# Performance work log

Measured on AMD Instinct MI355X. Metric: run time of the kernel, lower is better.

Reference implementation:

```python
import jax, jax.numpy as jnp
import numpy as np
from jax import lax


def setup_inputs() -> dict:
    key = jax.random.key(0)
    ks = jax.random.split(key, 16)
    B, T, F = 32, 32, 64
    H, N, A, C = 256, 1024, 64, 192
    M = A + C  # overall_memory_size
    s = 0.05  # weight scale (xavier-like magnitude)
    inp = {
        "batch": jax.random.normal(ks[0], (B, T, F), jnp.float32),
        "Wi": jax.random.normal(ks[1], (3, H, F), jnp.float32) * s,
        "bi": jax.random.normal(ks[2], (3, H, 1), jnp.float32) * s,
        "Wh": jax.random.normal(ks[3], (3, H, H), jnp.float32) * s,
        "bh": jax.random.normal(ks[4], (3, H, 1), jnp.float32) * s,
        "Wm": jax.random.normal(ks[5], (3, H, M), jnp.float32) * s,
        "bm": jax.random.normal(ks[6], (3, H, 1), jnp.float32) * s,
        "W_output": jax.random.normal(ks[7], (10, H), jnp.float32) * s,
        "b_output": jnp.full((10, 1), 0.1, jnp.float32),
        "memory_addresses": jax.random.normal(ks[8], (N, A), jnp.float32) * s,
        "W_query": jax.random.normal(ks[9], (M, H), jnp.float32) * s,
        "b_query": jax.random.normal(ks[10], (M, 1), jnp.float32) * s,
        "u_sharpen": jax.random.normal(ks[11], (1, H), jnp.float32) * s,
        "W_content_hidden": jax.random.normal(ks[12], (C, H), jnp.float32) * s,
        "W_content_input": jax.random.normal(ks[13], (C, F), jnp.float32) * s,
    }
    return inp


def reference(batch, Wi, bi, Wh, bh, Wm, bm, W_output, b_output,
              memory_addresses, W_query, b_query, u_sharpen,
              W_content_hidden, W_content_input):
    B, T, F = batch.shape
    H = Wh.shape[1]
    N, A = memory_addresses.shape
    C = W_content_hidden.shape[0]

    # faithful to torch: batch[:, t, :].reshape(F, B) per step (raw reshape, not transpose)
    xs = jnp.transpose(batch, (1, 0, 2)).reshape(T, F, B)  # [T, F, B]

    h0 = jnp.zeros((H, B), batch.dtype)
    content0 = jnp.zeros((B, N, C), batch.dtype)
    addr = jnp.broadcast_to(memory_addresses, (B, N, A))

    def step(carry, x):
        h, content = carry  # h: [H,B], content: [B,N,C]
        full = jnp.concatenate([addr, content], axis=-1)  # [B,N,M]
        # content-based addressing with sharpening
        q = W_query @ h + b_query                          # [M,B]
        sim = jnp.einsum('bnm,mb->nb', full, q)            # [N,B]
        beta = jax.nn.softplus(u_sharpen @ h) + 1.0        # [1,B]
        w = jax.nn.softmax(beta * sim, axis=0)             # [N,B]
        # read (before update, as in step_on_batch_element)
        reading = jnp.einsum('bnm,nb->mb', full, w)        # [M,B]
        # write: additive ReLU candidate
        cand = jax.nn.relu(W_content_hidden @ h + W_content_input @ x)  # [C,B]
        content = content + jnp.einsum('nb,cb->bnc', w, cand)
        # CustomGRU: gate order [r, z, n]
        gi = jnp.einsum('ghf,fb->ghb', Wi, x) + bi
        gh = jnp.einsum('ghk,kb->ghb', Wh, h) + bh
        gm = jnp.einsum('ghm,mb->ghb', Wm, reading) + bm
        r = jax.nn.sigmoid(gi[0] + gh[0] + gm[0])
        z = jax.nn.sigmoid(gi[1] + gh[1] + gm[1])
        n = jnp.tanh(gi[2] + gm[2] + r * gh[2])
        h_new = (1.0 - z) * n + z * h
        out = jax.nn.log_softmax(W_output @ h_new + b_output, axis=0)  # [10,B]
        return (h_new, content), (h_new, out)

    _, (hs, outs) = lax.scan(step, (h0, content0), xs)
    return hs, outs  # [T,H,B], [T,10,B]
```

## Files before the change

kernel.cpp:

```cpp
#include <hip/hip_runtime.h>

typedef unsigned int u32;
typedef unsigned short u16;
typedef _Float16 f16x2 __attribute__((ext_vector_type(2)));


#define WP_A0    0
#define WP_A1    40960
#define WP_A2H   81920
#define WP_A2I   114688
#define WP_AQ    122880
#define WP_AC    155648
#define WP_AM    186368
#define WP_AT2   284672
#define WP_M4    317440
#define WP_WO4   350208

#define SH_HX   0
#define SH_H2   256
#define SH_Q    416
#define SH_Q2   672
#define SH_GA0  704
#define SH_GA1  960
#define SH_GH2  1216
#define SH_GI2  1472
#define SH_GM   1728
#define SH_SIMA 2496
#define SH_R2   3520
#define SH_D    3648
#define SH_G    3680
#define SH_RED  3712
#define SH_RED2 3728
#define SH_MISC 3744
#define SH_B10  3752
#define SH_RA   3768
#define SH_CAND 4280
#define SH_W    7352
#define SMEM_FLOATS 23736
#define SMEM_BYTES (SMEM_FLOATS*4)

#define WRED(v) { v += __shfl_xor(v,32); v += __shfl_xor(v,16); v += __shfl_xor(v,8); \
                  v += __shfl_xor(v,4);  v += __shfl_xor(v,2);  v += __shfl_xor(v,1); }

__device__ __forceinline__ f16x2 bch2(u32 u) { return __builtin_bit_cast(f16x2, u); }

#if __has_builtin(__builtin_amdgcn_fdot2)
__device__ __forceinline__ float FDOT2(u32 a, u32 b, float c) {
  return __builtin_amdgcn_fdot2(bch2(a), bch2(b), c, false);
}
#else
__device__ __forceinline__ float FDOT2(u32 a, u32 b, float c) {
  f16x2 x = bch2(a), y = bch2(b);
  return c + (float)x[0]*(float)y[0] + (float)x[1]*(float)y[1];
}
#endif

__device__ __forceinline__ u16 f2h(float x) {
  _Float16 h = (_Float16)x; return __builtin_bit_cast(u16, h);
}
__device__ __forceinline__ float h2f(u16 u) {
  return (float)__builtin_bit_cast(_Float16, u);
}
__device__ __forceinline__ u32 packh2(float lo, float hi) {
  return (u32)f2h(lo) | ((u32)f2h(hi) << 16);
}

template<int NK4>
__device__ __forceinline__ float mv_os4(const u32* __restrict__ Wb,
                                        const u32* __restrict__ c2, const int ln)
{
  const uint4* wp = (const uint4*)Wb + ln;
  const uint4* c4 = (const uint4*)c2;
  uint4 w0 = wp[0], w1 = wp[64];
  uint4 c0 = c4[0], c1 = c4[1];
  wp += 128;
  float a0 = 0.f, a1 = 0.f, a2 = 0.f, a3 = 0.f;
  #pragma unroll 1
  for (int it = 0; it < NK4/2 - 1; ++it) {
    const uint4 nw0 = wp[0], nw1 = wp[64];
    const uint4 nc0 = c4[2*it + 2], nc1 = c4[2*it + 3];
    wp += 128;
    a0 = FDOT2(w0.x, c0.x, a0);
    a1 = FDOT2(w0.y, c0.y, a1);
    a2 = FDOT2(w0.z, c0.z, a2);
    a3 = FDOT2(w0.w, c0.w, a3);
    a0 = FDOT2(w1.x, c1.x, a0);
    a1 = FDOT2(w1.y, c1.y, a1);
    a2 = FDOT2(w1.z, c1.z, a2);
    a3 = FDOT2(w1.w, c1.w, a3);
    w0 = nw0; w1 = nw1; c0 = nc0; c1 = nc1;
  }
  a0 = FDOT2(w0.x, c0.x, a0);
  a1 = FDOT2(w0.y, c0.y, a1);
  a2 = FDOT2(w0.z, c0.z, a2);
  a3 = FDOT2(w0.w, c0.w, a3);
  a0 = FDOT2(w1.x, c1.x, a0);
  a1 = FDOT2(w1.y, c1.y, a1);
  a2 = FDOT2(w1.z, c1.z, a2);
  a3 = FDOT2(w1.w, c1.w, a3);
  return (a0 + a1) + (a2 + a3);
}

__device__ __forceinline__ void out_lse(const float* __restrict__ b10,
    float* __restrict__ out, const int t_out, const int bb, const int ln)
{
  float v = (ln < 10) ? b10[ln] : -1e30f;
  float m = v;
  m = fmaxf(m, __shfl_xor(m, 8, 16));
  m = fmaxf(m, __shfl_xor(m, 4, 16));
  m = fmaxf(m, __shfl_xor(m, 2, 16));
  m = fmaxf(m, __shfl_xor(m, 1, 16));
  float e = (ln < 10) ? __expf(v - m) : 0.f;
  float s = e;
  s += __shfl_xor(s, 8, 16);
  s += __shfl_xor(s, 4, 16);
  s += __shfl_xor(s, 2, 16);
  s += __shfl_xor(s, 1, 16);
  if (ln < 10) out[262144 + t_out * 320 + ln * 32 + bb] = v - m - logf(s);
}

__device__ __forceinline__ void pack_panel(const float* __restrict__ srcA, int KA, int np4A,
                                           const float* __restrict__ srcB, int KB,
                                           int np4tot, int o0, u32* __restrict__ dstu, int tid)
{
  uint4* d4 = (uint4*)dstu;
  for (int idx = tid; idx < np4tot * 64; idx += 256) {
    const int k4 = idx >> 6, o = idx & 63;
    const float* s = (k4 < np4A) ? (srcA + (size_t)(o0 + o) * KA + k4 * 8)
                                 : (srcB + (size_t)(o0 + o) * KB + (k4 - np4A) * 8);
    uint4 v;
    v.x = packh2(s[0], s[1]); v.y = packh2(s[2], s[3]);
    v.z = packh2(s[4], s[5]); v.w = packh2(s[6], s[7]);
    d4[idx] = v;
  }
}

__global__ void pack_weights(const float* __restrict__ Wi, const float* __restrict__ Wh,
                             const float* __restrict__ Wm, const float* __restrict__ Wq,
                             const float* __restrict__ Wch, const float* __restrict__ Wci,
                             const float* __restrict__ maddr, const float* __restrict__ Wo,
                             u32* __restrict__ wsu)
{
  const int b = blockIdx.x, tid = threadIdx.x;
  if (b < 4)        pack_panel(Wh,          256, 32, Wi,        64, 40, b*64,      wsu + WP_A0  + b*10240, tid);
  else if (b < 8)   pack_panel(Wh + 65536,  256, 32, Wi + 16384,64, 40, (b-4)*64,  wsu + WP_A1  + (b-4)*10240, tid);
  else if (b < 12)  pack_panel(Wh + 131072, 256, 32, Wh,       256, 32, (b-8)*64,  wsu + WP_A2H + (b-8)*8192, tid);
  else if (b < 16)  pack_panel(Wi + 32768,   64,  8, Wi,        64,  8, (b-12)*64, wsu + WP_A2I + (b-12)*2048, tid);
  else if (b < 20)  pack_panel(Wq,          256, 32, Wq,       256, 32, (b-16)*64, wsu + WP_AQ  + (b-16)*8192, tid);
  else if (b < 23)  pack_panel(Wch,         256, 32, Wci,       64, 40, (b-20)*64, wsu + WP_AC  + (b-20)*10240, tid);
  else if (b < 35) { int x = b-23; int g = x>>2;
                    pack_panel(Wm + g*65536, 256, 32, Wm,      256, 32, (x&3)*64,  wsu + WP_AM  + x*8192, tid); }
  else if (b < 51)  pack_panel(maddr,        64,  8, maddr,     64,  8, (b-35)*64, wsu + WP_AT2 + (b-35)*2048, tid);
  else if (b < 55) {
    const int kb = b - 51;
    uint4* d4 = (uint4*)(wsu + WP_M4);
    for (int idx = tid; idx < 2048; idx += 256) {
      const int k4 = kb*32 + (idx >> 6), a = idx & 63;
      const float* s = maddr + (size_t)(8*k4)*64 + a;
      uint4 v;
      v.x = packh2(s[0],   s[64]);  v.y = packh2(s[128], s[192]);
      v.z = packh2(s[256], s[320]); v.w = packh2(s[384], s[448]);
      d4[k4*64 + a] = v;
    }
  } else {
    uint4* d4 = (uint4*)(wsu + WP_WO4);
    for (int idx = tid; idx < 320; idx += 256) {
      const int j = idx >> 5, l = idx & 31;
      const float* s = Wo + j*256 + l*8;
      uint4 v;
      v.x = packh2(s[0], s[1]); v.y = packh2(s[2], s[3]);
      v.z = packh2(s[4], s[5]); v.w = packh2(s[6], s[7]);
      d4[idx] = v;
    }
  }
}

__global__ __launch_bounds__(1024) void dntm_step(
    const float* __restrict__ batch, const float* __restrict__ bi,
    const float* __restrict__ bh, const float* __restrict__ bm,
    const float* __restrict__ bo, const float* __restrict__ bq,
    const float* __restrict__ usharp, const u32* __restrict__ wsu,
    float* __restrict__ out)
{
  extern __shared__ float sm[];
  u32* h2u   = (u32*)(sm + SH_H2);
  u32* Q2u   = (u32*)(sm + SH_Q2);
  u32* R2u   = (u32*)(sm + SH_R2);
  u16* candh = (u16*)(sm + SH_CAND);
  u16* SW16  = (u16*)(sm + SH_W);
  u32* SW32  = (u32*)(sm + SH_W);
  const int tid = threadIdx.x, ln = tid & 63, wv = tid >> 6;
  const int bb = blockIdx.x;

  if (tid < 256) sm[SH_HX + tid] = 0.f;
  if (tid < 128) h2u[tid] = 0u;
  if (tid >= 128 && tid < 160) {
    const int j = tid - 128;
    const int i0 = (2*j)*32 + bb, i1 = i0 + 32;
    const float x0 = batch[(i0 >> 6)*2048 + (i0 & 63)];
    const float x1 = batch[(i1 >> 6)*2048 + (i1 & 63)];
    h2u[128 + j] = packh2(x0, x1);
  }
  __syncthreads();

  for (int t = 0; t < 32; ++t) {
    if (wv < 4) {
      sm[SH_GA0 + wv*64 + ln] = mv_os4<40>(wsu + WP_A0 + wv*10240, h2u, ln);
    } else if (wv < 8) {
      const int p = wv - 4;
      sm[SH_GA1 + p*64 + ln] = mv_os4<40>(wsu + WP_A1 + p*10240, h2u, ln);
    } else if (wv < 12) {
      const int p = wv - 8;
      sm[SH_GH2 + p*64 + ln] = mv_os4<32>(wsu + WP_A2H + p*8192, h2u, ln);
      sm[SH_GI2 + p*64 + ln] = mv_os4<8> (wsu + WP_A2I + p*2048, h2u + 128, ln);
    } else if (wv == 12) {
      const float qa = mv_os4<32>(wsu + WP_AQ,        h2u, ln) + bq[ln];
      const float qb = mv_os4<32>(wsu + WP_AQ + 8192, h2u, ln) + bq[64 + ln];
      sm[SH_Q + ln] = qa; sm[SH_Q + 64 + ln] = qb;
      const float rh = __shfl_down(qa, 1);
      if (!(ln & 1)) Q2u[ln >> 1] = packh2(qa, rh);
    } else if (wv == 13) {
      sm[SH_Q + 128 + ln] = mv_os4<32>(wsu + WP_AQ + 16384, h2u, ln) + bq[128 + ln];
      sm[SH_Q + 192 + ln] = mv_os4<32>(wsu + WP_AQ + 24576, h2u, ln) + bq[192 + ln];
    } else if (wv == 14) {
      candh[t*192 +      ln] = f2h(fmaxf(mv_os4<40>(wsu + WP_AC,         h2u, ln), 0.f));
      candh[t*192 + 64 + ln] = f2h(fmaxf(mv_os4<40>(wsu + WP_AC + 10240, h2u, ln), 0.f));
    } else {
      candh[t*192 + 128 + ln] = f2h(fmaxf(mv_os4<40>(wsu + WP_AC + 20480, h2u, ln), 0.f));
      {
        const float4 h4 = *(const float4*)(sm + SH_HX + ln*4);
        const float4 u4 = *(const float4*)(usharp + ln*4);
        float v = h4.x*u4.x + h4.y*u4.y + h4.z*u4.z + h4.w*u4.w;
        WRED(v);
        if (!ln) sm[SH_MISC] = fmaxf(v, 0.f) + log1pf(expf(-fabsf(v))) + 1.f;
      }
      if (t > 0) {
        const uint4 ch = ((const uint4*)h2u)[ln & 31];
        const uint4* wo4 = (const uint4*)(wsu + WP_WO4);
        for (int j = 0; j < 10; ++j) {
          float lv = 0.f;
          if (ln < 32) {
            const uint4 w4 = wo4[j*32 + ln];
            lv = FDOT2(w4.x, ch.x, lv); lv = FDOT2(w4.y, ch.y, lv);
            lv = FDOT2(w4.z, ch.z, lv); lv = FDOT2(w4.w, ch.w, lv);
          }
          WRED(lv);
          if (!ln) sm[SH_B10 + j] = lv + bo[j];
        }
      }
    }
    __syncthreads();

    if (wv < 8) {
      sm[SH_SIMA + wv*128 + ln]      = mv_os4<8>(wsu + WP_AT2 + (2*wv)*2048,   Q2u, ln);
      sm[SH_SIMA + wv*128 + 64 + ln] = mv_os4<8>(wsu + WP_AT2 + (2*wv+1)*2048, Q2u, ln);
    } else if (wv < 15) {
      const float q0 = sm[SH_Q + 64 + ln], q1 = sm[SH_Q + 128 + ln], q2 = sm[SH_Q + 192 + ln];
      for (int s = wv - 8; s < t; s += 7) {
        float a2 = h2f(candh[s*192 + ln]) * q0
                 + h2f(candh[s*192 + 64 + ln]) * q1
                 + h2f(candh[s*192 + 128 + ln]) * q2;
        WRED(a2);
        if (!ln) sm[SH_D + s] = a2;
      }
    } else {
      if (t > 0) out_lse(sm + SH_B10, out, t - 1, bb, ln);
    }
    __syncthreads();

    const int n3 = wv * 64 + ln;
    float v = sm[SH_SIMA + n3];
    #pragma unroll 4
    for (int s = 0; s < t; ++s) v = fmaf(sm[SH_D + s], h2f(SW16[s*1024 + n3]), v);
    v *= sm[SH_MISC];
    {
      float mx = v;
      mx = fmaxf(mx, __shfl_xor(mx, 32)); mx = fmaxf(mx, __shfl_xor(mx, 16));
      mx = fmaxf(mx, __shfl_xor(mx, 8));  mx = fmaxf(mx, __shfl_xor(mx, 4));
      mx = fmaxf(mx, __shfl_xor(mx, 2));  mx = fmaxf(mx, __shfl_xor(mx, 1));
      if (!ln) sm[SH_RED + wv] = mx;
    }
    __syncthreads();

    {
      float gmx = sm[SH_RED];
      #pragma unroll
      for (int i = 1; i < 16; ++i) gmx = fmaxf(gmx, sm[SH_RED + i]);
      const float e = __expf(v - gmx);
      SW16[t*1024 + n3] = f2h(e);
      float s2 = e; WRED(s2);
      if (!ln) sm[SH_RED2 + wv] = s2;
    }
    __syncthreads();

    {
      float tot = 0.f;
      #pragma unroll
      for (int i = 0; i < 16; ++i) tot += sm[SH_RED2 + i];
      const float inv = 1.0f / tot;
      if (wv < 8) {
        const float acc = mv_os4<16>(wsu + WP_M4 + wv*16*256,
                                     SW32 + t*512 + wv*64, ln);
        sm[SH_RA + wv*64 + ln] = acc * inv;
      } else {
        const uint4 ea = ((const uint4*)(SW32 + t*512))[ln*2];
        const uint4 eb = ((const uint4*)(SW32 + t*512))[ln*2 + 1];
        for (int s = wv - 8; s < t; s += 8) {
          const uint4 wa = ((const uint4*)(SW32 + s*512))[ln*2];
          const uint4 wb = ((const uint4*)(SW32 + s*512))[ln*2 + 1];
          float a2 = 0.f;
          a2 = FDOT2(ea.x, wa.x, a2); a2 = FDOT2(ea.y, wa.y, a2);
          a2 = FDOT2(ea.z, wa.z, a2); a2 = FDOT2(ea.w, wa.w, a2);
          a2 = FDOT2(eb.x, wb.x, a2); a2 = FDOT2(eb.y, wb.y, a2);
          a2 = FDOT2(eb.z, wb.z, a2); a2 = FDOT2(eb.w, wb.w, a2);
          WRED(a2);
          if (!ln) sm[SH_G + s] = a2 * inv;
        }
      }
    }
    __syncthreads();

    if (wv == 0) {
      float r = 0.f;
      #pragma unroll
      for (int j = 0; j < 8; ++j) r += sm[SH_RA + j*64 + ln];
      const float rh = __shfl_down(r, 1);
      if (!(ln & 1)) R2u[ln >> 1] = packh2(r, rh);
    } else if (wv < 4) {
      const int c = (wv - 1)*64 + ln;
      float r = 0.f;
      for (int s = 0; s < t; ++s) r = fmaf(h2f(candh[s*192 + c]), sm[SH_G + s], r);
      const float rh = __shfl_down(r, 1);
      if (!(ln & 1)) R2u[wv*32 + (ln >> 1)] = packh2(r, rh);
    }
    __syncthreads();

    if (wv < 12) {
      const int g = wv >> 2, p = wv & 3;
      sm[SH_GM + g*256 + p*64 + ln] = mv_os4<32>(wsu + WP_AM + wv*8192, R2u, ln);
    } else if (wv < 14) {
      float tot = 0.f;
      #pragma unroll
      for (int i = 0; i < 16; ++i) tot += sm[SH_RED2 + i];
      const float inv = 1.0f / tot;
      u32* p = SW32 + t*512 + (wv - 12)*256 + ln*4;
      uint4 v4 = *(const uint4*)p;
      v4.x = packh2(h2f(v4.x & 0xffff)*inv, h2f(v4.x >> 16)*inv);
      v4.y = packh2(h2f(v4.y & 0xffff)*inv, h2f(v4.y >> 16)*inv);
      v4.z = packh2(h2f(v4.z & 0xffff)*inv, h2f(v4.z >> 16)*inv);
      v4.w = packh2(h2f(v4.w & 0xffff)*inv, h2f(v4.w >> 16)*inv);
      *(uint4*)p = v4;
    } else if (wv == 14) {
      if (t < 31 && ln < 32) {
        const int i0 = (2*ln)*32 + bb, i1 = i0 + 32;
        const float x0 = batch[(i0 >> 6)*2048 + (t+1)*64 + (i0 & 63)];
        const float x1 = batch[(i1 >> 6)*2048 + (t+1)*64 + (i1 & 63)];
        h2u[128 + ln] = packh2(x0, x1);
      }
    }
    __syncthreads();

    if (tid < 256) {
      const int h = tid;
      const float g0  = sm[SH_GA0 + h] + bi[h]       + bh[h]       + sm[SH_GM + h]       + bm[h];
      const float g1  = sm[SH_GA1 + h] + bi[256 + h] + bh[256 + h] + sm[SH_GM + 256 + h] + bm[256 + h];
      const float gh2v = sm[SH_GH2 + h] + bh[512 + h];
      const float gi2v = sm[SH_GI2 + h] + bi[512 + h];
      const float gm2  = sm[SH_GM + 512 + h] + bm[512 + h];
      const float r = 1.f / (1.f + __expf(-g0));
      const float z = 1.f / (1.f + __expf(-g1));
      const float nn = tanhf(gi2v + gm2 + r * gh2v);
      const float hn = (1.f - z) * nn + z * sm[SH_HX + h];
      sm[SH_HX + h] = hn;
      out[t*8192 + h*32 + bb] = hn;
      const float hn1 = __shfl_down(hn, 1);
      if (!(tid & 1)) h2u[tid >> 1] = packh2(hn, hn1);
    }
    __syncthreads();
  }

  if (wv == 0) {
    const uint4 ch = ((const uint4*)h2u)[ln & 31];
    const uint4* wo4 = (const uint4*)(wsu + WP_WO4);
    for (int j = 0; j < 10; ++j) {
      float lv = 0.f;
      if (ln < 32) {
        const uint4 w4 = wo4[j*32 + ln];
        lv = FDOT2(w4.x, ch.x, lv); lv = FDOT2(w4.y, ch.y, lv);
        lv = FDOT2(w4.z, ch.z, lv); lv = FDOT2(w4.w, ch.w, lv);
      }
      WRED(lv);
      if (!ln) sm[SH_B10 + j] = lv + bo[j];
    }
    out_lse(sm + SH_B10, out, 31, bb, ln);
  }
}

extern "C" void kernel_launch(void* const* d_in, const int* in_sizes, int n_in,
                              void* d_out, int out_size, void* d_ws, size_t ws_size,
                              hipStream_t stream) {
  (void)in_sizes; (void)n_in; (void)out_size; (void)ws_size;
  const float* batch = (const float*)d_in[0];
  const float* Wi    = (const float*)d_in[1];
  const float* bi    = (const float*)d_in[2];
  const float* Wh    = (const float*)d_in[3];
  const float* bh    = (const float*)d_in[4];
  const float* Wm    = (const float*)d_in[5];
  const float* bm    = (const float*)d_in[6];
  const float* Wo    = (const float*)d_in[7];
  const float* bo    = (const float*)d_in[8];
  const float* maddr = (const float*)d_in[9];
  const float* Wq    = (const float*)d_in[10];
  const float* bq    = (const float*)d_in[11];
  const float* us    = (const float*)d_in[12];
  const float* Wch   = (const float*)d_in[13];
  const float* Wci   = (const float*)d_in[14];
  u32* wsu  = (u32*)d_ws;
  float* out = (float*)d_out;

  hipFuncSetAttribute((const void*)dntm_step,
                      hipFuncAttributeMaxDynamicSharedMemorySize, 163840);

  pack_weights<<<56, 256, 0, stream>>>(Wi, Wh, Wm, Wq, Wch, Wci, maddr, Wo, wsu);
  dntm_step<<<32, 1024, SMEM_BYTES, stream>>>(batch, bi, bh, bm, bo, bq, us, wsu, out);
}
```

Before: 585.1 us.

## Rebalance per-wave matvec work and deepen load pipelining in fp16 dot helpers

Reassigns the first-phase matvecs across the 16 waves. The Wh n-gate product is split in two K-halves, spread over waves 0-7 and summed in the GRU stage. The candidate, query, input-gate and output-logit work is regrouped so no wave carries two full 40-group matvecs. The mv_os4 helper is fully unrolled with double-buffered groups of four uint4 loads, and a paired helper does two 8-group matvecs with interleaved loads. The goal is a shorter critical path per timestep, at the cost of more registers and an extra shared-memory partial buffer, with a launch-bounds hint added.

```diff
diff --git a/kernel.cpp b/kernel.cpp
--- a/kernel.cpp
+++ b/kernel.cpp
@@ -16,27 +16,28 @@
 #define WP_M4    317440
 #define WP_WO4   350208
 
-#define SH_HX   0
-#define SH_H2   256
-#define SH_Q    416
-#define SH_Q2   672
-#define SH_GA0  704
-#define SH_GA1  960
-#define SH_GH2  1216
-#define SH_GI2  1472
-#define SH_GM   1728
-#define SH_SIMA 2496
-#define SH_R2   3520
-#define SH_D    3648
-#define SH_G    3680
-#define SH_RED  3712
-#define SH_RED2 3728
-#define SH_MISC 3744
-#define SH_B10  3752
-#define SH_RA   3768
-#define SH_CAND 4280
-#define SH_W    7352
-#define SMEM_FLOATS 23736
+#define SH_HX    0
+#define SH_H2    256
+#define SH_Q     416
+#define SH_Q2    672
+#define SH_GA0   704
+#define SH_GA1   960
+#define SH_GH2A  1216
+#define SH_GH2B  1472
+#define SH_GI2   1728
+#define SH_GM    1984
+#define SH_SIMA  2752
+#define SH_R2    3776
+#define SH_D     3904
+#define SH_G     3936
+#define SH_RED   3968
+#define SH_RED2  3984
+#define SH_MISC  4000
+#define SH_B10   4008
+#define SH_RA    4024
+#define SH_CAND  4536
+#define SH_W     7608
+#define SMEM_FLOATS 23992
 #define SMEM_BYTES (SMEM_FLOATS*4)
 
 #define WRED(v) { v += __shfl_xor(v,32); v += __shfl_xor(v,16); v += __shfl_xor(v,8); \
@@ -69,36 +70,75 @@
 __device__ __forceinline__ float mv_os4(const u32* __restrict__ Wb,
                                         const u32* __restrict__ c2, const int ln)
 {
-  const uint4* wp = (const uint4*)Wb + ln;
-  const uint4* c4 = (const uint4*)c2;
-  uint4 w0 = wp[0], w1 = wp[64];
-  uint4 c0 = c4[0], c1 = c4[1];
-  wp += 128;
+  static_assert(NK4 % 4 == 0, "NK4 must be multiple of 4");
+  constexpr int NG = NK4 / 4;
+  const uint4* __restrict__ wp = (const uint4*)Wb + ln;
+  const uint4* __restrict__ c4 = (const uint4*)c2;
   float a0 = 0.f, a1 = 0.f, a2 = 0.f, a3 = 0.f;
-  #pragma unroll 1
-  for (int it = 0; it < NK4/2 - 1; ++it) {
-    const uint4 nw0 = wp[0], nw1 = wp[64];
-    const uint4 nc0 = c4[2*it + 2], nc1 = c4[2*it + 3];
-    wp += 128;
-    a0 = FDOT2(w0.x, c0.x, a0);
-    a1 = FDOT2(w0.y, c0.y, a1);
-    a2 = FDOT2(w0.z, c0.z, a2);
-    a3 = FDOT2(w0.w, c0.w, a3);
-    a0 = FDOT2(w1.x, c1.x, a0);
-    a1 = FDOT2(w1.y, c1.y, a1);
-    a2 = FDOT2(w1.z, c1.z, a2);
-    a3 = FDOT2(w1.w, c1.w, a3);
-    w0 = nw0; w1 = nw1; c0 = nc0; c1 = nc1;
-  }
-  a0 = FDOT2(w0.x, c0.x, a0);
-  a1 = FDOT2(w0.y, c0.y, a1);
-  a2 = FDOT2(w0.z, c0.z, a2);
-  a3 = FDOT2(w0.w, c0.w, a3);
-  a0 = FDOT2(w1.x, c1.x, a0);
-  a1 = FDOT2(w1.y, c1.y, a1);
-  a2 = FDOT2(w1.z, c1.z, a2);
-  a3 = FDOT2(w1.w, c1.w, a3);
+  uint4 wa0, wa1, wa2, wa3, ca0, ca1, ca2, ca3;
+  uint4 wb0, wb1, wb2, wb3, cb0, cb1, cb2, cb3;
+#define LWA_(g) { wa0 = wp[(g)*256]; wa1 = wp[(g)*256+64]; wa2 = wp[(g)*256+128]; wa3 = wp[(g)*256+192]; \
+                  ca0 = c4[(g)*4];   ca1 = c4[(g)*4+1];    ca2 = c4[(g)*4+2];     ca3 = c4[(g)*4+3]; }
+#define LWB_(g) { wb0 = wp[(g)*256]; wb1 = wp[(g)*256+64]; wb2 = wp[(g)*256+128]; wb3 = wp[(g)*256+192]; \
+                  cb0 = c4[(g)*4];   cb1 = c4[(g)*4+1];    cb2 = c4[(g)*4+2];     cb3 = c4[(g)*4+3]; }
+#define CMPA_ { a0=FDOT2(wa0.x,ca0.x,a0); a1=FDOT2(wa0.y,ca0.y,a1); a2=FDOT2(wa0.z,ca0.z,a2); a3=FDOT2(wa0.w,ca0.w,a3); \
+                a0=FDOT2(wa1.x,ca1.x,a0); a1=FDOT2(wa1.y,ca1.y,a1); a2=FDOT2(wa1.z,ca1.z,a2); a3=FDOT2(wa1.w,ca1.w,a3); \
+                a0=FDOT2(wa2.x,ca2.x,a0); a1=FDOT2(wa2.y,ca2.y,a1); a2=FDOT2(wa2.z,ca2.z,a2); a3=FDOT2(wa2.w,ca2.w,a3); \
+                a0=FDOT2(wa3.x,ca3.x,a0); a1=FDOT2(wa3.y,ca3.y,a1); a2=FDOT2(wa3.z,ca3.z,a2); a3=FDOT2(wa3.w,ca3.w,a3); }
+#define CMPB_ { a0=FDOT2(wb0.x,cb0.x,a0); a1=FDOT2(wb0.y,cb0.y,a1); a2=FDOT2(wb0.z,cb0.z,a2); a3=FDOT2(wb0.w,cb0.w,a3); \
+                a0=FDOT2(wb1.x,cb1.x,a0); a1=FDOT2(wb1.y,cb1.y,a1); a2=FDOT2(wb1.z,cb1.z,a2); a3=FDOT2(wb1.w,cb1.w,a3); \
+                a0=FDOT2(wb2.x,cb2.x,a0); a1=FDOT2(wb2.y,cb2.y,a1); a2=FDOT2(wb2.z,cb2.z,a2); a3=FDOT2(wb2.w,cb2.w,a3); \
+                a0=FDOT2(wb3.x,cb3.x,a0); a1=FDOT2(wb3.y,cb3.y,a1); a2=FDOT2(wb3.z,cb3.z,a2); a3=FDOT2(wb3.w,cb3.w,a3); }
+  LWA_(0);
+  if constexpr (NG == 1) {
+    CMPA_;
+  } else {
+    LWB_(1);
+    #pragma unroll
+    for (int g = 0; g + 2 < NG; ++g) {
+      if ((g & 1) == 0) { CMPA_; LWA_(g + 2); }
+      else              { CMPB_; LWB_(g + 2); }
+    }
+    if constexpr (((NG - 2) & 1) == 0) { CMPA_; CMPB_; }
+    else                               { CMPB_; CMPA_; }
+  }
+#undef LWA_
+#undef LWB_
+#undef CMPA_
+#undef CMPB_
   return (a0 + a1) + (a2 + a3);
+}
+
+__device__ __forceinline__ float2 mv2_os4_8(const u32* __restrict__ W0,
+    const u32* __restrict__ W1, const u32* __restrict__ c2, const int ln)
+{
+  const uint4* __restrict__ w0p = (const uint4*)W0 + ln;
+  const uint4* __restrict__ w1p = (const uint4*)W1 + ln;
+  const uint4* __restrict__ c4 = (const uint4*)c2;
+  float a0=0.f,a1=0.f,a2=0.f,a3=0.f, b0=0.f,b1=0.f,b2=0.f,b3=0.f;
+  uint4 wa0=w0p[0],   wa1=w0p[64],  wa2=w0p[128], wa3=w0p[192];
+  uint4 ca0=c4[0],    ca1=c4[1],    ca2=c4[2],    ca3=c4[3];
+  uint4 wb0=w0p[256], wb1=w0p[320], wb2=w0p[384], wb3=w0p[448];
+  uint4 cb0=c4[4],    cb1=c4[5],    cb2=c4[6],    cb3=c4[7];
+  a0=FDOT2(wa0.x,ca0.x,a0); a1=FDOT2(wa0.y,ca0.y,a1); a2=FDOT2(wa0.z,ca0.z,a2); a3=FDOT2(wa0.w,ca0.w,a3);
+  a0=FDOT2(wa1.x,ca1.x,a0); a1=FDOT2(wa1.y,ca1.y,a1); a2=FDOT2(wa1.z,ca1.z,a2); a3=FDOT2(wa1.w,ca1.w,a3);
+  a0=FDOT2(wa2.x,ca2.x,a0); a1=FDOT2(wa2.y,ca2.y,a1); a2=FDOT2(wa2.z,ca2.z,a2); a3=FDOT2(wa2.w,ca2.w,a3);
+  a0=FDOT2(wa3.x,ca3.x,a0); a1=FDOT2(wa3.y,ca3.y,a1); a2=FDOT2(wa3.z,ca3.z,a2); a3=FDOT2(wa3.w,ca3.w,a3);
+  wa0=w1p[0]; wa1=w1p[64]; wa2=w1p[128]; wa3=w1p[192];
+  a0=FDOT2(wb0.x,cb0.x,a0); a1=FDOT2(wb0.y,cb0.y,a1); a2=FDOT2(wb0.z,cb0.z,a2); a3=FDOT2(wb0.w,cb0.w,a3);
+  a0=FDOT2(wb1.x,cb1.x,a0); a1=FDOT2(wb1.y,cb1.y,a1); a2=FDOT2(wb1.z,cb1.z,a2); a3=FDOT2(wb1.w,cb1.w,a3);
+  a0=FDOT2(wb2.x,cb2.x,a0); a1=FDOT2(wb2.y,cb2.y,a1); a2=FDOT2(wb2.z,cb2.z,a2); a3=FDOT2(wb2.w,cb2.w,a3);
+  a0=FDOT2(wb3.x,cb3.x,a0); a1=FDOT2(wb3.y,cb3.y,a1); a2=FDOT2(wb3.z,cb3.z,a2); a3=FDOT2(wb3.w,cb3.w,a3);
+  wb0=w1p[256]; wb1=w1p[320]; wb2=w1p[384]; wb3=w1p[448];
+  b0=FDOT2(wa0.x,ca0.x,b0); b1=FDOT2(wa0.y,ca0.y,b1); b2=FDOT2(wa0.z,ca0.z,b2); b3=FDOT2(wa0.w,ca0.w,b3);
+  b0=FDOT2(wa1.x,ca1.x,b0); b1=FDOT2(wa1.y,ca1.y,b1); b2=FDOT2(wa1.z,ca1.z,b2); b3=FDOT2(wa1.w,ca1.w,b3);
+  b0=FDOT2(wa2.x,ca2.x,b0); b1=FDOT2(wa2.y,ca2.y,b1); b2=FDOT2(wa2.z,ca2.z,b2); b3=FDOT2(wa2.w,ca2.w,b3);
+  b0=FDOT2(wa3.x,ca3.x,b0); b1=FDOT2(wa3.y,ca3.y,b1); b2=FDOT2(wa3.z,ca3.z,b2); b3=FDOT2(wa3.w,ca3.w,b3);
+  b0=FDOT2(wb0.x,cb0.x,b0); b1=FDOT2(wb0.y,cb0.y,b1); b2=FDOT2(wb0.z,cb0.z,b2); b3=FDOT2(wb0.w,cb0.w,b3);
+  b0=FDOT2(wb1.x,cb1.x,b0); b1=FDOT2(wb1.y,cb1.y,b1); b2=FDOT2(wb1.z,cb1.z,b2); b3=FDOT2(wb1.w,cb1.w,b3);
+  b0=FDOT2(wb2.x,cb2.x,b0); b1=FDOT2(wb2.y,cb2.y,b1); b2=FDOT2(wb2.z,cb2.z,b2); b3=FDOT2(wb2.w,cb2.w,b3);
+  b0=FDOT2(wb3.x,cb3.x,b0); b1=FDOT2(wb3.y,cb3.y,b1); b2=FDOT2(wb3.z,cb3.z,b2); b3=FDOT2(wb3.w,cb3.w,b3);
+  return make_float2((a0+a1)+(a2+a3), (b0+b1)+(b2+b3));
 }
 
 __device__ __forceinline__ void out_lse(const float* __restrict__ b10,
@@ -175,7 +215,7 @@
   }
 }
 
-__global__ __launch_bounds__(1024) void dntm_step(
+__global__ __launch_bounds__(1024, 4) void dntm_step(
     const float* __restrict__ batch, const float* __restrict__ bi,
     const float* __restrict__ bh, const float* __restrict__ bm,
     const float* __restrict__ bo, const float* __restrict__ bq,
@@ -204,29 +244,24 @@
   __syncthreads();
 
   for (int t = 0; t < 32; ++t) {
-    if (wv < 4) {
-      sm[SH_GA0 + wv*64 + ln] = mv_os4<40>(wsu + WP_A0 + wv*10240, h2u, ln);
-    } else if (wv < 8) {
-      const int p = wv - 4;
-      sm[SH_GA1 + p*64 + ln] = mv_os4<40>(wsu + WP_A1 + p*10240, h2u, ln);
-    } else if (wv < 12) {
+    if (wv < 8) {
+      if (wv < 4) {
+        sm[SH_GA0 + wv*64 + ln] = mv_os4<40>(wsu + WP_A0 + wv*10240, h2u, ln);
+      } else {
+        sm[SH_GA1 + (wv-4)*64 + ln] = mv_os4<40>(wsu + WP_A1 + (wv-4)*10240, h2u, ln);
+      }
+      const int p = wv >> 1, pt = wv & 1;
+      const float hv = mv_os4<16>(wsu + WP_A2H + p*8192 + pt*4096, h2u + pt*64, ln);
+      sm[(pt ? SH_GH2B : SH_GH2A) + p*64 + ln] = hv;
+    } else if (wv < 11) {
       const int p = wv - 8;
-      sm[SH_GH2 + p*64 + ln] = mv_os4<32>(wsu + WP_A2H + p*8192, h2u, ln);
-      sm[SH_GI2 + p*64 + ln] = mv_os4<8> (wsu + WP_A2I + p*2048, h2u + 128, ln);
-    } else if (wv == 12) {
-      const float qa = mv_os4<32>(wsu + WP_AQ,        h2u, ln) + bq[ln];
-      const float qb = mv_os4<32>(wsu + WP_AQ + 8192, h2u, ln) + bq[64 + ln];
-      sm[SH_Q + ln] = qa; sm[SH_Q + 64 + ln] = qb;
-      const float rh = __shfl_down(qa, 1);
-      if (!(ln & 1)) Q2u[ln >> 1] = packh2(qa, rh);
-    } else if (wv == 13) {
-      sm[SH_Q + 128 + ln] = mv_os4<32>(wsu + WP_AQ + 16384, h2u, ln) + bq[128 + ln];
-      sm[SH_Q + 192 + ln] = mv_os4<32>(wsu + WP_AQ + 24576, h2u, ln) + bq[192 + ln];
-    } else if (wv == 14) {
-      candh[t*192 +      ln] = f2h(fmaxf(mv_os4<40>(wsu + WP_AC,         h2u, ln), 0.f));
-      candh[t*192 + 64 + ln] = f2h(fmaxf(mv_os4<40>(wsu + WP_AC + 10240, h2u, ln), 0.f));
-    } else {
-      candh[t*192 + 128 + ln] = f2h(fmaxf(mv_os4<40>(wsu + WP_AC + 20480, h2u, ln), 0.f));
+      const float cv = mv_os4<40>(wsu + WP_AC + p*10240, h2u, ln);
+      candh[t*192 + p*64 + ln] = f2h(fmaxf(cv, 0.f));
+    } else if (wv == 11) {
+      const float2 r01 = mv2_os4_8(wsu+WP_A2I,        wsu+WP_A2I+2048, h2u+128, ln);
+      const float2 r23 = mv2_os4_8(wsu+WP_A2I+4096,   wsu+WP_A2I+6144, h2u+128, ln);
+      sm[SH_GI2 +       ln] = r01.x; sm[SH_GI2 +  64 + ln] = r01.y;
+      sm[SH_GI2 + 128 + ln] = r23.x; sm[SH_GI2 + 192 + ln] = r23.y;
       {
         const float4 h4 = *(const float4*)(sm + SH_HX + ln*4);
         const float4 u4 = *(const float4*)(usharp + ln*4);
@@ -234,7 +269,15 @@
         WRED(v);
         if (!ln) sm[SH_MISC] = fmaxf(v, 0.f) + log1pf(expf(-fabsf(v))) + 1.f;
       }
-      if (t > 0) {
+    } else {
+      const int p = wv - 12;
+      const float qv = mv_os4<32>(wsu + WP_AQ + p*8192, h2u, ln) + bq[p*64 + ln];
+      sm[SH_Q + p*64 + ln] = qv;
+      if (wv == 12) {
+        const float qh = __shfl_down(qv, 1);
+        if (!(ln & 1)) Q2u[ln >> 1] = packh2(qv, qh);
+      }
+      if (wv == 13 && t > 0) {
         const uint4 ch = ((const uint4*)h2u)[ln & 31];
         const uint4* wo4 = (const uint4*)(wsu + WP_WO4);
         for (int j = 0; j < 10; ++j) {
@@ -252,8 +295,10 @@
     __syncthreads();
 
     if (wv < 8) {
-      sm[SH_SIMA + wv*128 + ln]      = mv_os4<8>(wsu + WP_AT2 + (2*wv)*2048,   Q2u, ln);
-      sm[SH_SIMA + wv*128 + 64 + ln] = mv_os4<8>(wsu + WP_AT2 + (2*wv+1)*2048, Q2u, ln);
+      const float2 r = mv2_os4_8(wsu + WP_AT2 + (2*wv)*2048,
+                                 wsu + WP_AT2 + (2*wv+1)*2048, Q2u, ln);
+      sm[SH_SIMA + wv*128 + ln]      = r.x;
+      sm[SH_SIMA + wv*128 + 64 + ln] = r.y;
     } else if (wv < 15) {
       const float q0 = sm[SH_Q + 64 + ln], q1 = sm[SH_Q + 128 + ln], q2 = sm[SH_Q + 192 + ln];
       for (int s = wv - 8; s < t; s += 7) {
@@ -364,7 +409,7 @@
       const int h = tid;
       const float g0  = sm[SH_GA0 + h] + bi[h]       + bh[h]       + sm[SH_GM + h]       + bm[h];
       const float g1  = sm[SH_GA1 + h] + bi[256 + h] + bh[256 + h] + sm[SH_GM + 256 + h] + bm[256 + h];
-      const float gh2v = sm[SH_GH2 + h] + bh[512 + h];
+      const float gh2v = sm[SH_GH2A + h] + sm[SH_GH2B + h] + bh[512 + h];
       const float gi2v = sm[SH_GI2 + h] + bi[512 + h];
       const float gm2  = sm[SH_GM + 512 + h] + bm[512 + h];
       const float r = 1.f / (1.f + __expf(-g0));
```

New measurement: 1.353 ms. 131% more time.

## Quantize recurrent weight panels to per-row uint8 with fp16 dot decode

Applied to the files above, without the earlier changes.

Weight panels are now packed as per-output-row asymmetric uint8 with a scale and offset, in place of fp16. The matvecs decode bytes into fp16 through the 0x6400 magic-number trick and apply the scale and offset using a running sum of the input vector. This halves the weight bytes streamed from global memory on every timestep. Wave roles are also rebalanced: the candidate matvec moves to the second phase and the query work is spread over four waves. The cost is lower weight precision, which may increase error, and extra decode ALU work per element.

```diff
diff --git a/kernel.cpp b/kernel.cpp
--- a/kernel.cpp
+++ b/kernel.cpp
@@ -6,36 +6,47 @@
 
 
 #define WP_A0    0
-#define WP_A1    40960
-#define WP_A2H   81920
-#define WP_A2I   114688
-#define WP_AQ    122880
-#define WP_AC    155648
-#define WP_AM    186368
-#define WP_AT2   284672
-#define WP_M4    317440
-#define WP_WO4   350208
-
-#define SH_HX   0
-#define SH_H2   256
-#define SH_Q    416
-#define SH_Q2   672
-#define SH_GA0  704
-#define SH_GA1  960
-#define SH_GH2  1216
-#define SH_GI2  1472
-#define SH_GM   1728
-#define SH_SIMA 2496
-#define SH_R2   3520
-#define SH_D    3648
-#define SH_G    3680
-#define SH_RED  3712
-#define SH_RED2 3728
-#define SH_MISC 3744
-#define SH_B10  3752
-#define SH_RA   3768
-#define SH_CAND 4280
-#define SH_W    7352
+#define WP_A1    20480
+#define WP_A2H   40960
+#define WP_A2I   57344
+#define WP_AQ    61440
+#define WP_AC    77824
+#define WP_AM    93184
+#define WP_AT2   142336
+#define WP_M4    158720
+#define WP_WO4   175104
+#define WP_SC    176384
+
+#define SC_A0   0
+#define SC_A1   256
+#define SC_A2H  512
+#define SC_A2I  768
+#define SC_AQ   1024
+#define SC_AC   1280
+#define SC_AM   1472
+#define SC_AT2  2240
+#define SC_M4   3264
+
+#define SH_HX    0
+#define SH_H2    256
+#define SH_Q     416
+#define SH_Q2    672
+#define SH_GA0   704
+#define SH_GA1   960
+#define SH_GH2   1216
+#define SH_GI2   1472
+#define SH_GM    1728
+#define SH_SIMA  2496
+#define SH_R2    3520
+#define SH_D     3648
+#define SH_G     3680
+#define SH_RED   3712
+#define SH_RED2  3728
+#define SH_MISC  3744
+#define SH_B10   3752
+#define SH_RA    3768
+#define SH_CAND  4280
+#define SH_W     7352
 #define SMEM_FLOATS 23736
 #define SMEM_BYTES (SMEM_FLOATS*4)
 
@@ -65,40 +76,51 @@
   return (u32)f2h(lo) | ((u32)f2h(hi) << 16);
 }
 
-template<int NK4>
-__device__ __forceinline__ float mv_os4(const u32* __restrict__ Wb,
-                                        const u32* __restrict__ c2, const int ln)
+#define ONE2 0x3C003C00u
+
+template<int J>
+__device__ __forceinline__ u32 mkpair(u32 w) {
+#if __has_builtin(__builtin_amdgcn_perm)
+  const u32 sel = (J == 0) ? 0x0C010C00u : 0x0C030C02u;
+  return __builtin_amdgcn_perm(w, w, sel) | 0x64006400u;
+#else
+  return (((w >> (8*J)) & 0xFFu) | (((w >> (8*J + 8)) & 0xFFu) << 16)) | 0x64006400u;
+#endif
+}
+
+template<int NK16, int MODE>
+__device__ __forceinline__ float mv_u8(const u32* __restrict__ Wb,
+    const u32* __restrict__ c2, const float2* __restrict__ scale, const int ln)
 {
-  const uint4* wp = (const uint4*)Wb + ln;
-  const uint4* c4 = (const uint4*)c2;
-  uint4 w0 = wp[0], w1 = wp[64];
-  uint4 c0 = c4[0], c1 = c4[1];
-  wp += 128;
-  float a0 = 0.f, a1 = 0.f, a2 = 0.f, a3 = 0.f;
-  #pragma unroll 1
-  for (int it = 0; it < NK4/2 - 1; ++it) {
-    const uint4 nw0 = wp[0], nw1 = wp[64];
-    const uint4 nc0 = c4[2*it + 2], nc1 = c4[2*it + 3];
-    wp += 128;
-    a0 = FDOT2(w0.x, c0.x, a0);
-    a1 = FDOT2(w0.y, c0.y, a1);
-    a2 = FDOT2(w0.z, c0.z, a2);
-    a3 = FDOT2(w0.w, c0.w, a3);
-    a0 = FDOT2(w1.x, c1.x, a0);
-    a1 = FDOT2(w1.y, c1.y, a1);
-    a2 = FDOT2(w1.z, c1.z, a2);
-    a3 = FDOT2(w1.w, c1.w, a3);
-    w0 = nw0; w1 = nw1; c0 = nc0; c1 = nc1;
-  }
-  a0 = FDOT2(w0.x, c0.x, a0);
-  a1 = FDOT2(w0.y, c0.y, a1);
-  a2 = FDOT2(w0.z, c0.z, a2);
-  a3 = FDOT2(w0.w, c0.w, a3);
-  a0 = FDOT2(w1.x, c1.x, a0);
-  a1 = FDOT2(w1.y, c1.y, a1);
-  a2 = FDOT2(w1.z, c1.z, a2);
-  a3 = FDOT2(w1.w, c1.w, a3);
-  return (a0 + a1) + (a2 + a3);
+  const uint4* __restrict__ wp = (const uint4*)Wb + ln;
+  const uint4* __restrict__ c4 = (const uint4*)c2;
+  uint4 w[4];
+  #pragma unroll
+  for (int i = 0; i < 4; ++i) if (i < NK16) w[i] = wp[i*64];
+  float a0 = 0.f, a1 = 0.f, a2 = 0.f, a3 = 0.f, s0 = 0.f, s1 = 0.f;
+  #pragma unroll
+  for (int i = 0; i < NK16; ++i) {
+    const uint4 cw0 = c4[2*i], cw1 = c4[2*i + 1];
+    const uint4 ww = w[i & 3];
+    if (i + 4 < NK16) w[i & 3] = wp[(i + 4)*64];
+    a0 = FDOT2(mkpair<0>(ww.x), cw0.x, a0);
+    a1 = FDOT2(mkpair<2>(ww.x), cw0.y, a1);
+    a2 = FDOT2(mkpair<0>(ww.y), cw0.z, a2);
+    a3 = FDOT2(mkpair<2>(ww.y), cw0.w, a3);
+    a0 = FDOT2(mkpair<0>(ww.z), cw1.x, a0);
+    a1 = FDOT2(mkpair<2>(ww.z), cw1.y, a1);
+    a2 = FDOT2(mkpair<0>(ww.w), cw1.z, a2);
+    a3 = FDOT2(mkpair<2>(ww.w), cw1.w, a3);
+    s0 = FDOT2(cw0.x, ONE2, s0); s1 = FDOT2(cw0.y, ONE2, s1);
+    s0 = FDOT2(cw0.z, ONE2, s0); s1 = FDOT2(cw0.w, ONE2, s1);
+    s0 = FDOT2(cw1.x, ONE2, s0); s1 = FDOT2(cw1.y, ONE2, s1);
+    s0 = FDOT2(cw1.z, ONE2, s0); s1 = FDOT2(cw1.w, ONE2, s1);
+  }
+  const float dotq = (a0 + a1) + (a2 + a3);
+  const float sumc = s0 + s1;
+  if (MODE == 1) return dotq - 1024.0f*sumc;
+  const float2 sc = scale[ln];
+  return sc.x*dotq + sc.y*sumc;
 }
 
 __device__ __forceinline__ void out_lse(const float* __restrict__ b10,
@@ -119,22 +141,6 @@
   if (ln < 10) out[262144 + t_out * 320 + ln * 32 + bb] = v - m - logf(s);
 }
 
-__device__ __forceinline__ void pack_panel(const float* __restrict__ srcA, int KA, int np4A,
-                                           const float* __restrict__ srcB, int KB,
-                                           int np4tot, int o0, u32* __restrict__ dstu, int tid)
-{
-  uint4* d4 = (uint4*)dstu;
-  for (int idx = tid; idx < np4tot * 64; idx += 256) {
-    const int k4 = idx >> 6, o = idx & 63;
-    const float* s = (k4 < np4A) ? (srcA + (size_t)(o0 + o) * KA + k4 * 8)
-                                 : (srcB + (size_t)(o0 + o) * KB + (k4 - np4A) * 8);
-    uint4 v;
-    v.x = packh2(s[0], s[1]); v.y = packh2(s[2], s[3]);
-    v.z = packh2(s[4], s[5]); v.w = packh2(s[6], s[7]);
-    d4[idx] = v;
-  }
-}
-
 __global__ void pack_weights(const float* __restrict__ Wi, const float* __restrict__ Wh,
                              const float* __restrict__ Wm, const float* __restrict__ Wq,
                              const float* __restrict__ Wch, const float* __restrict__ Wci,
@@ -142,27 +148,7 @@
                              u32* __restrict__ wsu)
 {
   const int b = blockIdx.x, tid = threadIdx.x;
-  if (b < 4)        pack_panel(Wh,          256, 32, Wi,        64, 40, b*64,      wsu + WP_A0  + b*10240, tid);
-  else if (b < 8)   pack_panel(Wh + 65536,  256, 32, Wi + 16384,64, 40, (b-4)*64,  wsu + WP_A1  + (b-4)*10240, tid);
-  else if (b < 12)  pack_panel(Wh + 131072, 256, 32, Wh,       256, 32, (b-8)*64,  wsu + WP_A2H + (b-8)*8192, tid);
-  else if (b < 16)  pack_panel(Wi + 32768,   64,  8, Wi,        64,  8, (b-12)*64, wsu + WP_A2I + (b-12)*2048, tid);
-  else if (b < 20)  pack_panel(Wq,          256, 32, Wq,       256, 32, (b-16)*64, wsu + WP_AQ  + (b-16)*8192, tid);
-  else if (b < 23)  pack_panel(Wch,         256, 32, Wci,       64, 40, (b-20)*64, wsu + WP_AC  + (b-20)*10240, tid);
-  else if (b < 35) { int x = b-23; int g = x>>2;
-                    pack_panel(Wm + g*65536, 256, 32, Wm,      256, 32, (x&3)*64,  wsu + WP_AM  + x*8192, tid); }
-  else if (b < 51)  pack_panel(maddr,        64,  8, maddr,     64,  8, (b-35)*64, wsu + WP_AT2 + (b-35)*2048, tid);
-  else if (b < 55) {
-    const int kb = b - 51;
-    uint4* d4 = (uint4*)(wsu + WP_M4);
-    for (int idx = tid; idx < 2048; idx += 256) {
-      const int k4 = kb*32 + (idx >> 6), a = idx & 63;
-      const float* s = maddr + (size_t)(8*k4)*64 + a;
-      uint4 v;
-      v.x = packh2(s[0],   s[64]);  v.y = packh2(s[128], s[192]);
-      v.z = packh2(s[256], s[320]); v.w = packh2(s[384], s[448]);
-      d4[k4*64 + a] = v;
-    }
-  } else {
+  if (b == 52) {
     uint4* d4 = (uint4*)(wsu + WP_WO4);
     for (int idx = tid; idx < 320; idx += 256) {
       const int j = idx >> 5, l = idx & 31;
@@ -172,6 +158,69 @@
       v.z = packh2(s[4], s[5]); v.w = packh2(s[6], s[7]);
       d4[idx] = v;
     }
+    return;
+  }
+  const float *srcA = nullptr, *srcB = nullptr;
+  int KA = 0, KB = 0, Ktot = 0, o0 = 0, scb = 0;
+  u32* dst = nullptr; bool colmode = false, m4mode = false;
+  if (b < 4)       { srcA=Wh;         KA=256; srcB=Wi;         KB=64; Ktot=320; o0=b*64;
+                     dst=wsu+WP_A0 + b*5120;       scb=SC_A0  + b*64; }
+  else if (b < 8)  { srcA=Wh+65536;   KA=256; srcB=Wi+16384;   KB=64; Ktot=320; o0=(b-4)*64;
+                     dst=wsu+WP_A1 + (b-4)*5120;   scb=SC_A1  + (b-4)*64; }
+  else if (b < 12) { srcA=Wh+131072;  KA=256; Ktot=256; o0=(b-8)*64;
+                     dst=wsu+WP_A2H + (b-8)*4096;  scb=SC_A2H + (b-8)*64; }
+  else if (b < 16) { srcA=Wi+32768;   KA=64;  Ktot=64;  o0=(b-12)*64;
+                     dst=wsu+WP_A2I + (b-12)*1024; scb=SC_A2I + (b-12)*64; }
+  else if (b < 20) { srcA=Wq;         KA=256; Ktot=256; o0=(b-16)*64;
+                     dst=wsu+WP_AQ + (b-16)*4096;  scb=SC_AQ  + (b-16)*64; }
+  else if (b < 23) { srcA=Wch;        KA=256; srcB=Wci;        KB=64; Ktot=320; o0=(b-20)*64;
+                     dst=wsu+WP_AC + (b-20)*5120;  scb=SC_AC  + (b-20)*64; }
+  else if (b < 35) { const int x = b-23;
+                     srcA=Wm + (x>>2)*65536; KA=256; Ktot=256; o0=(x&3)*64;
+                     dst=wsu+WP_AM + x*4096;       scb=SC_AM  + x*64; }
+  else if (b < 51) { srcA=maddr;      KA=64;  Ktot=64;  o0=(b-35)*64;
+                     dst=wsu+WP_AT2 + (b-35)*1024; scb=SC_AT2 + (b-35)*64; }
+  else             { srcA=maddr;      KA=1024; Ktot=1024; o0=0; colmode=true; m4mode=true;
+                     dst=wsu+WP_M4;                scb=SC_M4; }
+
+  const int o = tid & 63, q = tid >> 6;
+  const int kq = Ktot >> 2;
+  float mn = 3e38f, mx = -3e38f;
+  for (int k = q*kq; k < (q+1)*kq; ++k) {
+    const float v = colmode ? srcA[(size_t)k*64 + o]
+                  : ((k < KA) ? srcA[(size_t)(o0+o)*KA + k]
+                              : srcB[(size_t)(o0+o)*KB + (k - KA)]);
+    mn = fminf(mn, v); mx = fmaxf(mx, v);
+  }
+  __shared__ float smn[4][64], smx[4][64], sS[64], sMu[64];
+  smn[q][o] = mn; smx[q][o] = mx;
+  __syncthreads();
+  if (tid < 64) {
+    mn = fminf(fminf(smn[0][tid], smn[1][tid]), fminf(smn[2][tid], smn[3][tid]));
+    mx = fmaxf(fmaxf(smx[0][tid], smx[1][tid]), fmaxf(smx[2][tid], smx[3][tid]));
+    const float s = fmaxf((mx - mn)*(1.0f/255.0f), 1e-20f);
+    const float mu = 0.5f*(mx + mn);
+    sS[tid] = s; sMu[tid] = mu;
+    float2* scp = (float2*)(wsu + WP_SC) + scb + tid;
+    *scp = make_float2(s, m4mode ? (128.0f*s - mu) : (mu - 1152.0f*s));
+  }
+  __syncthreads();
+  const float s = sS[o], mu = sMu[o], rs = 1.0f/s;
+  uint4* d4 = (uint4*)dst;
+  for (int cc = q*(kq >> 4); cc < (q+1)*(kq >> 4); ++cc) {
+    u32 wd0 = 0, wd1 = 0, wd2 = 0, wd3 = 0;
+    #pragma unroll
+    for (int j = 0; j < 16; ++j) {
+      const int k = cc*16 + j;
+      const float v = colmode ? srcA[(size_t)k*64 + o]
+                    : ((k < KA) ? srcA[(size_t)(o0+o)*KA + k]
+                                : srcB[(size_t)(o0+o)*KB + (k - KA)]);
+      const u32 bq8 = (u32)(int)fminf(fmaxf(rintf((v - mu)*rs) + 128.0f, 0.0f), 255.0f);
+      const u32 sh = (u32)((j & 3)*8);
+      if (j < 4) wd0 |= bq8 << sh; else if (j < 8) wd1 |= bq8 << sh;
+      else if (j < 12) wd2 |= bq8 << sh; else wd3 |= bq8 << sh;
+    }
+    d4[cc*64 + o] = make_uint4(wd0, wd1, wd2, wd3);
   }
 }
 
@@ -189,6 +238,7 @@
   u16* candh = (u16*)(sm + SH_CAND);
   u16* SW16  = (u16*)(sm + SH_W);
   u32* SW32  = (u32*)(sm + SH_W);
+  const float2* SC = (const float2*)(wsu + WP_SC);
   const int tid = threadIdx.x, ln = tid & 63, wv = tid >> 6;
   const int bb = blockIdx.x;
 
@@ -205,36 +255,28 @@
 
   for (int t = 0; t < 32; ++t) {
     if (wv < 4) {
-      sm[SH_GA0 + wv*64 + ln] = mv_os4<40>(wsu + WP_A0 + wv*10240, h2u, ln);
+      sm[SH_GA0 + wv*64 + ln] = mv_u8<20,0>(wsu + WP_A0 + wv*5120, h2u, SC + SC_A0 + wv*64, ln);
     } else if (wv < 8) {
       const int p = wv - 4;
-      sm[SH_GA1 + p*64 + ln] = mv_os4<40>(wsu + WP_A1 + p*10240, h2u, ln);
+      sm[SH_GA1 + p*64 + ln] = mv_u8<20,0>(wsu + WP_A1 + p*5120, h2u, SC + SC_A1 + p*64, ln);
     } else if (wv < 12) {
       const int p = wv - 8;
-      sm[SH_GH2 + p*64 + ln] = mv_os4<32>(wsu + WP_A2H + p*8192, h2u, ln);
-      sm[SH_GI2 + p*64 + ln] = mv_os4<8> (wsu + WP_A2I + p*2048, h2u + 128, ln);
-    } else if (wv == 12) {
-      const float qa = mv_os4<32>(wsu + WP_AQ,        h2u, ln) + bq[ln];
-      const float qb = mv_os4<32>(wsu + WP_AQ + 8192, h2u, ln) + bq[64 + ln];
-      sm[SH_Q + ln] = qa; sm[SH_Q + 64 + ln] = qb;
-      const float rh = __shfl_down(qa, 1);
-      if (!(ln & 1)) Q2u[ln >> 1] = packh2(qa, rh);
-    } else if (wv == 13) {
-      sm[SH_Q + 128 + ln] = mv_os4<32>(wsu + WP_AQ + 16384, h2u, ln) + bq[128 + ln];
-      sm[SH_Q + 192 + ln] = mv_os4<32>(wsu + WP_AQ + 24576, h2u, ln) + bq[192 + ln];
-    } else if (wv == 14) {
-      candh[t*192 +      ln] = f2h(fmaxf(mv_os4<40>(wsu + WP_AC,         h2u, ln), 0.f));
-      candh[t*192 + 64 + ln] = f2h(fmaxf(mv_os4<40>(wsu + WP_AC + 10240, h2u, ln), 0.f));
+      sm[SH_GH2 + p*64 + ln] = mv_u8<16,0>(wsu + WP_A2H + p*4096, h2u, SC + SC_A2H + p*64, ln);
+      sm[SH_GI2 + p*64 + ln] = mv_u8<4,0>(wsu + WP_A2I + p*1024, h2u + 128, SC + SC_A2I + p*64, ln);
     } else {
-      candh[t*192 + 128 + ln] = f2h(fmaxf(mv_os4<40>(wsu + WP_AC + 20480, h2u, ln), 0.f));
-      {
+      const int p = wv - 12;
+      const float qv = mv_u8<16,0>(wsu + WP_AQ + p*4096, h2u, SC + SC_AQ + p*64, ln) + bq[p*64 + ln];
+      sm[SH_Q + p*64 + ln] = qv;
+      if (wv == 12) {
+        const float qh = __shfl_down(qv, 1);
+        if (!(ln & 1)) Q2u[ln >> 1] = packh2(qv, qh);
         const float4 h4 = *(const float4*)(sm + SH_HX + ln*4);
         const float4 u4 = *(const float4*)(usharp + ln*4);
         float v = h4.x*u4.x + h4.y*u4.y + h4.z*u4.z + h4.w*u4.w;
         WRED(v);
         if (!ln) sm[SH_MISC] = fmaxf(v, 0.f) + log1pf(expf(-fabsf(v))) + 1.f;
       }
-      if (t > 0) {
+      if (wv == 13 && t > 0) {
         const uint4 ch = ((const uint4*)h2u)[ln & 31];
         const uint4* wo4 = (const uint4*)(wsu + WP_WO4);
         for (int j = 0; j < 10; ++j) {
@@ -252,11 +294,17 @@
     __syncthreads();
 
     if (wv < 8) {
-      sm[SH_SIMA + wv*128 + ln]      = mv_os4<8>(wsu + WP_AT2 + (2*wv)*2048,   Q2u, ln);
-      sm[SH_SIMA + wv*128 + 64 + ln] = mv_os4<8>(wsu + WP_AT2 + (2*wv+1)*2048, Q2u, ln);
+      sm[SH_SIMA + wv*128 + ln] =
+        mv_u8<4,0>(wsu + WP_AT2 + (2*wv)*1024, Q2u, SC + SC_AT2 + (2*wv)*64, ln);
+      sm[SH_SIMA + wv*128 + 64 + ln] =
+        mv_u8<4,0>(wsu + WP_AT2 + (2*wv + 1)*1024, Q2u, SC + SC_AT2 + (2*wv + 1)*64, ln);
+    } else if (wv < 11) {
+      const int p = wv - 8;
+      const float cv = mv_u8<20,0>(wsu + WP_AC + p*5120, h2u, SC + SC_AC + p*64, ln);
+      candh[t*192 + p*64 + ln] = f2h(fmaxf(cv, 0.f));
     } else if (wv < 15) {
       const float q0 = sm[SH_Q + 64 + ln], q1 = sm[SH_Q + 128 + ln], q2 = sm[SH_Q + 192 + ln];
-      for (int s = wv - 8; s < t; s += 7) {
+      for (int s = wv - 11; s < t; s += 4) {
         float a2 = h2f(candh[s*192 + ln]) * q0
                  + h2f(candh[s*192 + 64 + ln]) * q1
                  + h2f(candh[s*192 + 128 + ln]) * q2;
@@ -293,37 +341,40 @@
     }
     __syncthreads();
 
-    {
+    if (wv < 8) {
+      sm[SH_RA + wv*64 + ln] =
+        mv_u8<8,1>(wsu + WP_M4 + wv*2048, SW32 + t*512 + wv*64, nullptr, ln);
+    } else {
       float tot = 0.f;
       #pragma unroll
       for (int i = 0; i < 16; ++i) tot += sm[SH_RED2 + i];
       const float inv = 1.0f / tot;
-      if (wv < 8) {
-        const float acc = mv_os4<16>(wsu + WP_M4 + wv*16*256,
-                                     SW32 + t*512 + wv*64, ln);
-        sm[SH_RA + wv*64 + ln] = acc * inv;
-      } else {
-        const uint4 ea = ((const uint4*)(SW32 + t*512))[ln*2];
-        const uint4 eb = ((const uint4*)(SW32 + t*512))[ln*2 + 1];
-        for (int s = wv - 8; s < t; s += 8) {
-          const uint4 wa = ((const uint4*)(SW32 + s*512))[ln*2];
-          const uint4 wb = ((const uint4*)(SW32 + s*512))[ln*2 + 1];
-          float a2 = 0.f;
-          a2 = FDOT2(ea.x, wa.x, a2); a2 = FDOT2(ea.y, wa.y, a2);
-          a2 = FDOT2(ea.z, wa.z, a2); a2 = FDOT2(ea.w, wa.w, a2);
-          a2 = FDOT2(eb.x, wb.x, a2); a2 = FDOT2(eb.y, wb.y, a2);
-          a2 = FDOT2(eb.z, wb.z, a2); a2 = FDOT2(eb.w, wb.w, a2);
-          WRED(a2);
-          if (!ln) sm[SH_G + s] = a2 * inv;
-        }
+      const uint4 ea = ((const uint4*)(SW32 + t*512))[ln*2];
+      const uint4 eb = ((const uint4*)(SW32 + t*512))[ln*2 + 1];
+      for (int s = wv - 8; s < t; s += 8) {
+        const uint4 wa = ((const uint4*)(SW32 + s*512))[ln*2];
+        const uint4 wb = ((const uint4*)(SW32 + s*512))[ln*2 + 1];
+        float a2 = 0.f;
+        a2 = FDOT2(ea.x, wa.x, a2); a2 = FDOT2(ea.y, wa.y, a2);
+        a2 = FDOT2(ea.z, wa.z, a2); a2 = FDOT2(ea.w, wa.w, a2);
+        a2 = FDOT2(eb.x, wb.x, a2); a2 = FDOT2(eb.y, wb.y, a2);
+        a2 = FDOT2(eb.z, wb.z, a2); a2 = FDOT2(eb.w, wb.w, a2);
+        WRED(a2);
+        if (!ln) sm[SH_G + s] = a2 * inv;
       }
     }
     __syncthreads();
 
     if (wv == 0) {
-      float r = 0.f;
+      float tot = 0.f;
       #pragma unroll
-      for (int j = 0; j < 8; ++j) r += sm[SH_RA + j*64 + ln];
+      for (int i = 0; i < 16; ++i) tot += sm[SH_RED2 + i];
+      const float inv = 1.0f / tot;
+      float rsum = 0.f;
+      #pragma unroll
+      for (int j = 0; j < 8; ++j) rsum += sm[SH_RA + j*64 + ln];
+      const float2 sc = SC[SC_M4 + ln];
+      const float r = sc.x * (rsum * inv) - sc.y;
       const float rh = __shfl_down(r, 1);
       if (!(ln & 1)) R2u[ln >> 1] = packh2(r, rh);
     } else if (wv < 4) {
@@ -337,7 +388,8 @@
 
     if (wv < 12) {
       const int g = wv >> 2, p = wv & 3;
-      sm[SH_GM + g*256 + p*64 + ln] = mv_os4<32>(wsu + WP_AM + wv*8192, R2u, ln);
+      sm[SH_GM + g*256 + p*64 + ln] =
+        mv_u8<16,0>(wsu + WP_AM + wv*4096, R2u, SC + SC_AM + wv*64, ln);
     } else if (wv < 14) {
       float tot = 0.f;
       #pragma unroll
@@ -362,8 +414,8 @@
 
     if (tid < 256) {
       const int h = tid;
-      const float g0  = sm[SH_GA0 + h] + bi[h]       + bh[h]       + sm[SH_GM + h]       + bm[h];
-      const float g1  = sm[SH_GA1 + h] + bi[256 + h] + bh[256 + h] + sm[SH_GM + 256 + h] + bm[256 + h];
+      const float g0 = sm[SH_GA0 + h] + bi[h]       + bh[h]       + sm[SH_GM + h]       + bm[h];
+      const float g1 = sm[SH_GA1 + h] + bi[256 + h] + bh[256 + h] + sm[SH_GM + 256 + h] + bm[256 + h];
       const float gh2v = sm[SH_GH2 + h] + bh[512 + h];
       const float gi2v = sm[SH_GI2 + h] + bi[512 + h];
       const float gm2  = sm[SH_GM + 512 + h] + bm[512 + h];
@@ -421,6 +473,6 @@
   hipFuncSetAttribute((const void*)dntm_step,
                       hipFuncAttributeMaxDynamicSharedMemorySize, 163840);
 
-  pack_weights<<<56, 256, 0, stream>>>(Wi, Wh, Wm, Wq, Wch, Wci, maddr, Wo, wsu);
+  pack_weights<<<53, 256, 0, stream>>>(Wi, Wh, Wm, Wq, Wch, Wci, maddr, Wo, wsu);
   dntm_step<<<32, 1024, SMEM_BYTES, stream>>>(batch, bi, bh, bm, bo, bq, us, wsu, out);
 }
```

New measurement: 934.4 us. 1.6x slower.
